# Performance work log

Hardware: AMD Instinct MI355X
Metric: run time of the kernel (lower is better)

The kernel has to match this reference:

```python
import jax, jax.numpy as jnp
import numpy as np
from jax import lax

# Faithful JAX port of the approxmatch CUDA kernel (Fan et al. EMD):
#   iterates annealing levels j = 7 .. -2 with level = -4^j (0 at j=-2),
#   alternately normalizing transport weights by remaining source capacity
#   (remainL) and capping by remaining target capacity (remainR).
# Cost = sum over matched pairs of Euclidean (sqrt) distance * match weight.

def _approx_match(xyz1, xyz2):
    # xyz1: (b,n,3), xyz2: (b,m,3)
    b, n, _ = xyz1.shape
    m = xyz2.shape[1]
    # squared pairwise distances (b,n,m) -- computed once, reused every level
    d2 = jnp.sum((xyz1[:, :, None, :] - xyz2[:, None, :, :]) ** 2, axis=-1)
    # CUDA kernel capacities: multiL = max(1, m/n), multiR = max(1, n/m) (int ratios)
    multiL = float(max(1, m // n))
    multiR = float(max(1, n // m))
    remainL = jnp.full((b, n), multiL, dtype=xyz1.dtype)
    remainR = jnp.full((b, m), multiR, dtype=xyz1.dtype)
    match = jnp.zeros((b, n, m), dtype=xyz1.dtype)

    # levels for j = 7..-1 are -4^j; j = -2 uses level = 0
    levels = jnp.concatenate([
        -(4.0 ** jnp.arange(7, -2, -1, dtype=jnp.float32)),
        jnp.zeros((1,), jnp.float32),
    ])

    def body(carry, level):
        match, remainL, remainR = carry
        w = jnp.exp(level * d2) * remainR[:, None, :]                 # (b,n,m)
        w = w * (remainL / (1e-9 + w.sum(axis=2)))[:, :, None]        # normalize rows, scale by L capacity
        r = jnp.minimum(remainR / (1e-9 + w.sum(axis=1)), 1.0)        # cap columns by R capacity
        w = w * r[:, None, :]
        match = match + w
        remainL = jnp.maximum(remainL - w.sum(axis=2), 0.0)
        remainR = jnp.maximum(remainR - w.sum(axis=1), 0.0)
        return (match, remainL, remainR), None

    (match, _, _), _ = lax.scan(body, (match, remainL, remainR), levels)
    return match, d2


def _match_cost(match, d2):
    # matchcost kernel: sum_{k,l} match[k,l] * sqrt(||xyz1_k - xyz2_l||^2)
    dist = jnp.sqrt(jnp.maximum(d2, 1e-30))
    return jnp.sum(match * dist, axis=(1, 2))  # (b,)


def setup_inputs() -> dict:
    key = jax.random.key(0)
    k1, k2 = jax.random.split(key)
    b, n, m = 8, 2048, 2048
    input1 = jax.random.uniform(k1, (b, n, 3), dtype=jnp.float32)
    input2 = jax.random.uniform(k2, (b, m, 3), dtype=jnp.float32)
    return {"input1": input1, "input2": input2}


def reference(input1, input2):
    match, d2 = _approx_match(input1, input2)
    return _match_cost(match, d2)  # (b,) per-batch EMD cost
```

## Files before the change

### kernel.cpp

```cpp
#include <hip/hip_runtime.h>
#include <math.h>


#define NPTS 2048
#define BLOCK 256
#define RPB 16
#define L2E 1.4426950408889634f

typedef float v2 __attribute__((ext_vector_type(2)));

__device__ __forceinline__ float fexp2(float x) { return __builtin_amdgcn_exp2f(x); }
__device__ __forceinline__ float fsqrt(float x) { return __builtin_amdgcn_sqrtf(x); }
__device__ __forceinline__ v2 fma2(v2 a, v2 b, v2 c) { return __builtin_elementwise_fma(a, b, c); }
__device__ __forceinline__ v2 sp(float a) { v2 r; r.x = a; r.y = a; return r; }
__device__ __forceinline__ float xreduce(float v) {
#pragma unroll
    for (int off = 1; off < 64; off <<= 1) v += __shfl_xor(v, off, 64);
    return v;
}

struct RowPair { v2 pa, px, py, pz; };
__device__ __forceinline__ RowPair mk_pair(float4 a, float4 b, float kp) {
    RowPair r;
    r.pa = v2{kp * a.w, kp * b.w};
    r.px = v2{-2.f*kp*a.x, -2.f*kp*b.x};
    r.py = v2{-2.f*kp*a.y, -2.f*kp*b.y};
    r.pz = v2{-2.f*kp*a.z, -2.f*kp*b.z};
    return r;
}
__device__ __forceinline__ v2 term(const RowPair& r, float qx, float qy, float qz, v2 qb2) {
    return fma2(r.px, sp(qx), fma2(r.py, sp(qy), fma2(r.pz, sp(qz), r.pa + qb2)));
}

__global__ __launch_bounds__(BLOCK) void k_A(
    const float* __restrict__ xyz1, const float* __restrict__ xyz2,
    float4* __restrict__ p1w, float4* __restrict__ p2w,
    float* __restrict__ f_g, float kk, float multiL, float multiR)
{
    __shared__ float4 sQ[NPTS];
    const int row0 = blockIdx.x * RPB;
    const int batch = row0 >> 11;
    const int rloc = row0 & 2047;
    const float* g1 = xyz1 + (size_t)batch * NPTS * 3;
    const float* g2 = xyz2 + (size_t)batch * NPTS * 3;
    if (threadIdx.x < RPB) {
        int i = rloc + threadIdx.x;
        p1w[((size_t)batch << 11) + i] = make_float4(g1[3*i], g1[3*i+1], g1[3*i+2], 0.f);
    } else if (threadIdx.x < 2 * RPB) {
        int i = rloc + threadIdx.x - RPB;
        p2w[((size_t)batch << 11) + i] = make_float4(g2[3*i], g2[3*i+1], g2[3*i+2], 0.f);
    }
    for (int j = threadIdx.x; j < NPTS; j += BLOCK) {
        float qx = g2[3*j], qy = g2[3*j+1], qz = g2[3*j+2];
        sQ[j] = make_float4(qx, qy, qz, kk * (qx*qx + qy*qy + qz*qz));
    }
    __syncthreads();
    const int lane = threadIdx.x & 63;
    const int wave = threadIdx.x >> 6;
    const int r0 = row0 + wave * 4;
    RowPair rA, rB;
    {
        const float* p = g1 + 3 * (r0 & 2047);
        float4 p0 = make_float4(p[0], p[1], p[2], p[0]*p[0]+p[1]*p[1]+p[2]*p[2]);
        float4 p1 = make_float4(p[3], p[4], p[5], p[3]*p[3]+p[4]*p[4]+p[5]*p[5]);
        float4 p2 = make_float4(p[6], p[7], p[8], p[6]*p[6]+p[7]*p[7]+p[8]*p[8]);
        float4 p3 = make_float4(p[9], p[10], p[11], p[9]*p[9]+p[10]*p[10]+p[11]*p[11]);
        rA = mk_pair(p0, p1, kk); rB = mk_pair(p2, p3, kk);
    }
    v2 aSA = sp(0.f), aSB = sp(0.f);
#pragma unroll 8
    for (int j = lane; j < NPTS; j += 64) {
        float4 q = sQ[j];
        v2 qb2 = sp(q.w);
        v2 tA = term(rA, q.x, q.y, q.z, qb2);
        v2 tB = term(rB, q.x, q.y, q.z, qb2);
        aSA += v2{fexp2(tA.x), fexp2(tA.y)};
        aSB += v2{fexp2(tB.x), fexp2(tB.y)};
    }
    float sv[4] = {xreduce(aSA.x), xreduce(aSA.y), xreduce(aSB.x), xreduce(aSB.y)};
    if (lane == 0) {
#pragma unroll
        for (int r = 0; r < 4; ++r)
            f_g[r0 + r] = multiL / (1e-9f + multiR * sv[r]);
    }
}

template <bool FIRST>
__global__ __launch_bounds__(BLOCK) void k_B(
    const float4* __restrict__ p1w, const float4* __restrict__ p2w,
    const float* __restrict__ f_g, float* __restrict__ remR,
    float* __restrict__ c_g, float kk, float multiR)
{
    __shared__ float4 sQ[NPTS];
    __shared__ float sF[NPTS];
    const int col0 = blockIdx.x * RPB;
    const int batch = col0 >> 11;
    const float4* P1 = p1w + ((size_t)batch << 11);
    const float* F = f_g + ((size_t)batch << 11);
    for (int i = threadIdx.x; i < NPTS; i += BLOCK) {
        float4 q = P1[i];
        q.w = kk * (q.x*q.x + q.y*q.y + q.z*q.z);
        sQ[i] = q;
        sF[i] = F[i];
    }
    __syncthreads();
    const int lane = threadIdx.x & 63;
    const int wave = threadIdx.x >> 6;
    const int c0 = col0 + wave * 4;
    RowPair rA, rB;
    {
        float4 q0 = p2w[c0], q1 = p2w[c0+1], q2 = p2w[c0+2], q3 = p2w[c0+3];
        q0.w = q0.x*q0.x + q0.y*q0.y + q0.z*q0.z;
        q1.w = q1.x*q1.x + q1.y*q1.y + q1.z*q1.z;
        q2.w = q2.x*q2.x + q2.y*q2.y + q2.z*q2.z;
        q3.w = q3.x*q3.x + q3.y*q3.y + q3.z*q3.z;
        rA = mk_pair(q0, q1, kk); rB = mk_pair(q2, q3, kk);
    }
    v2 aSA = sp(0.f), aSB = sp(0.f);
#pragma unroll 8
    for (int i = lane; i < NPTS; i += 64) {
        float4 p = sQ[i];
        v2 qb2 = sp(p.w);
        v2 w2 = sp(sF[i]);
        v2 tA = term(rA, p.x, p.y, p.z, qb2);
        v2 tB = term(rB, p.x, p.y, p.z, qb2);
        aSA = fma2(w2, v2{fexp2(tA.x), fexp2(tA.y)}, aSA);
        aSB = fma2(w2, v2{fexp2(tB.x), fexp2(tB.y)}, aSB);
    }
    float sv[4] = {xreduce(aSA.x), xreduce(aSA.y), xreduce(aSB.x), xreduce(aSB.y)};
    if (lane == 0) {
#pragma unroll
        for (int r = 0; r < 4; ++r) {
            int gj = c0 + r;
            float R = FIRST ? multiR : remR[gj];
            float colsum = R * sv[r];
            float rr = fminf(R / (1e-9f + colsum), 1.0f);
            c_g[gj] = R * rr;
            remR[gj] = fmaxf(R - colsum * rr, 0.f);
        }
    }
}

template <int MODE, bool FIRSTC>
__global__ __launch_bounds__(BLOCK) void k_CA(
    const float4* __restrict__ p1w, const float4* __restrict__ p2w,
    float* __restrict__ f_g, const float* __restrict__ c_g,
    const float* __restrict__ remR, float* __restrict__ remL,
    float* __restrict__ costrow, float kp, float rsqkp, float multiL)
{
    __shared__ float4 sQ[NPTS];
    __shared__ float2 sCR[NPTS];
    const int row0 = blockIdx.x * RPB;
    const int batch = row0 >> 11;
    const float4* P2 = p2w + ((size_t)batch << 11);
    const float* C = c_g + ((size_t)batch << 11);
    const float* R = remR + ((size_t)batch << 11);
    for (int j = threadIdx.x; j < NPTS; j += BLOCK) {
        float4 q = P2[j];
        q.w = kp * (q.x*q.x + q.y*q.y + q.z*q.z);
        sQ[j] = q;
        sCR[j] = make_float2(C[j], MODE ? R[j] : 0.f);
    }
    __syncthreads();
    const int lane = threadIdx.x & 63;
    const int wave = threadIdx.x >> 6;
    const int r0 = row0 + wave * 4;

    if (MODE == 0) {
        float px[4], py[4], pz[4], aU[4];
#pragma unroll
        for (int r = 0; r < 4; ++r) {
            float4 q = p1w[r0 + r];
            px[r] = q.x; py[r] = q.y; pz[r] = q.z; aU[r] = 0.f;
        }
        float aT = 0.f;
#pragma unroll 4
        for (int j = lane; j < NPTS; j += 64) {
            float4 q = sQ[j];
            float cw = sCR[j].x;
            aT += cw;
#pragma unroll
            for (int r = 0; r < 4; ++r) {
                float dx = px[r]-q.x, dy = py[r]-q.y, dz = pz[r]-q.z;
                float d2 = fmaf(dx, dx, fmaf(dy, dy, dz * dz));
                aU[r] = fmaf(cw, fsqrt(d2), aU[r]);
            }
        }
        float tt = xreduce(aT);
#pragma unroll
        for (int r = 0; r < 4; ++r) {
            float uu = xreduce(aU[r]);
            if (lane == 0) {
                int gi = r0 + r;
                float fi = f_g[gi];
                remL[gi] = fmaxf(remL[gi] - fi * tt, 0.f);
                costrow[gi] += fi * uu;
            }
        }
        return;
    }

    RowPair rA, rB;
    v2 fiA, fiB;
    {
        float4 p0 = p1w[r0], p1 = p1w[r0+1], p2 = p1w[r0+2], p3 = p1w[r0+3];
        p0.w = p0.x*p0.x + p0.y*p0.y + p0.z*p0.z;
        p1.w = p1.x*p1.x + p1.y*p1.y + p1.z*p1.z;
        p2.w = p2.x*p2.x + p2.y*p2.y + p2.z*p2.z;
        p3.w = p3.x*p3.x + p3.y*p3.y + p3.z*p3.z;
        rA = mk_pair(p0, p1, kp); rB = mk_pair(p2, p3, kp);
        fiA = v2{f_g[r0], f_g[r0+1]}; fiB = v2{f_g[r0+2], f_g[r0+3]};
    }
    v2 aTA = sp(0.f), aTB = sp(0.f), aUA = sp(0.f), aUB = sp(0.f);
    v2 aAA = sp(0.f), aAB = sp(0.f);
    float aAs = 0.f;
#pragma unroll 4
    for (int j = lane; j < NPTS; j += 64) {
        float4 q = sQ[j];
        float2 crj = sCR[j];
        v2 qb2 = sp(q.w);
        float cw = crj.x, rw = crj.y;
        v2 tA = term(rA, q.x, q.y, q.z, qb2);
        v2 tB = term(rB, q.x, q.y, q.z, qb2);
        v2 eA = v2{fexp2(tA.x), fexp2(tA.y)};
        v2 eB = v2{fexp2(tB.x), fexp2(tB.y)};
        v2 eCA, eCB;
        if (MODE == 1) {
            v2 e2A = eA * eA, e2B = eB * eB;
            eCA = sp(cw) * (e2A * e2A); eCB = sp(cw) * (e2B * e2B);
        } else {
            eCA = sp(cw) * eA; eCB = sp(cw) * eB;
        }
        aTA += eCA; aTB += eCB;
        v2 stA = v2{fsqrt(fabsf(tA.x)), fsqrt(fabsf(tA.y))};
        v2 stB = v2{fsqrt(fabsf(tB.x)), fsqrt(fabsf(tB.y))};
        aUA = fma2(eCA, stA, aUA); aUB = fma2(eCB, stB, aUB);
        if (MODE == 1) { aAA = fma2(sp(rw), eA, aAA); aAB = fma2(sp(rw), eB, aAB); }
        else           { aAs += rw; }
    }
    float aas = (MODE == 2) ? xreduce(aAs) : 0.f;
    float tt[4] = {xreduce(aTA.x), xreduce(aTA.y), xreduce(aTB.x), xreduce(aTB.y)};
    float uu[4] = {xreduce(aUA.x), xreduce(aUA.y), xreduce(aUB.x), xreduce(aUB.y)};
    float aav[4];
    if (MODE == 1) {
        aav[0] = xreduce(aAA.x); aav[1] = xreduce(aAA.y);
        aav[2] = xreduce(aAB.x); aav[3] = xreduce(aAB.y);
    } else {
        aav[0] = aav[1] = aav[2] = aav[3] = aas;
    }
    float fiv[4] = {fiA.x, fiA.y, fiB.x, fiB.y};
    if (lane == 0) {
#pragma unroll
        for (int r = 0; r < 4; ++r) {
            int gi = r0 + r;
            float rl0 = FIRSTC ? multiL : remL[gi];
            float rl = fmaxf(rl0 - fiv[r] * tt[r], 0.f);
            costrow[gi] = (FIRSTC ? 0.f : costrow[gi]) + fiv[r] * uu[r] * rsqkp;
            remL[gi] = rl;
            f_g[gi] = rl / (1e-9f + aav[r]);
        }
    }
}

__global__ void k_cost(const float* __restrict__ costrow,
                       float* __restrict__ out, int n) {
    __shared__ float wsum[BLOCK / 64];
    const float* cr = costrow + (size_t)blockIdx.x * n;
    float s = 0.f;
    for (int i = threadIdx.x; i < n; i += BLOCK) s += cr[i];
    s = xreduce(s);
    int wave = threadIdx.x >> 6, lane = threadIdx.x & 63;
    if (lane == 0) wsum[wave] = s;
    __syncthreads();
    if (threadIdx.x == 0) {
        float t = 0.f;
#pragma unroll
        for (int w = 0; w < BLOCK / 64; ++w) t += wsum[w];
        out[blockIdx.x] = t;
    }
}

extern "C" void kernel_launch(void* const* d_in, const int* in_sizes, int n_in,
                              void* d_out, int out_size, void* d_ws, size_t ws_size,
                              hipStream_t stream) {
    const float* xyz1 = (const float*)d_in[0];
    const float* xyz2 = (const float*)d_in[1];
    float* out = (float*)d_out;
    const int b = out_size;
    const int n = in_sizes[0] / (3 * b);
    const int m = in_sizes[1] / (3 * b);
    const int bn = b * n, bm = b * m;

    float4* p1w = (float4*)d_ws;
    float4* p2w = p1w + bn;
    float* remL    = (float*)(p2w + bm);
    float* remR    = remL + bn;
    float* f       = remR + bm;
    float* c       = f + bn;
    float* costrow = c + bm;

    const float multiL = (float)((m / n > 1) ? (m / n) : 1);
    const float multiR = (float)((n / m > 1) ? (n / m) : 1);

    dim3 g(bn / RPB), blk(BLOCK);
    const float kk0 = -16384.f * L2E;
    k_A<<<g, blk, 0, stream>>>(xyz1, xyz2, p1w, p2w, f, kk0, multiL, multiR);

    for (int t = 0; t < 10; ++t) {
        const float lvl = (t < 9) ? -exp2f(2.f * (float)(7 - t)) : 0.f;
        const float kk = lvl * L2E;
        if (t == 0)
            k_B<true><<<g, blk, 0, stream>>>(p1w, p2w, f, remR, c, kk, multiR);
        else
            k_B<false><<<g, blk, 0, stream>>>(p1w, p2w, f, remR, c, kk, multiR);

        if (t < 8) {
            const float kp = kk * 0.25f;
            const float rsq = 1.f / sqrtf(-kp);
            if (t == 0)
                k_CA<1, true><<<g, blk, 0, stream>>>(p1w, p2w, f, c, remR, remL,
                                                     costrow, kp, rsq, multiL);
            else
                k_CA<1, false><<<g, blk, 0, stream>>>(p1w, p2w, f, c, remR, remL,
                                                      costrow, kp, rsq, multiL);
        } else if (t == 8) {
            const float kp = -0.25f * L2E;
            const float rsq = 1.f / sqrtf(0.25f * L2E);
            k_CA<2, false><<<g, blk, 0, stream>>>(p1w, p2w, f, c, remR, remL,
                                                  costrow, kp, rsq, multiL);
        } else {
            k_CA<0, false><<<g, blk, 0, stream>>>(p1w, p2w, f, c, remR, remL,
                                                  costrow, 0.f, 1.f, multiL);
        }
    }
    k_cost<<<dim3(b), blk, 0, stream>>>(costrow, out, n);
}
```

Measured before the change: 280.2 us.

## Process eight rows per wave with software-prefetched LDS loads

Each wave now handles 8 rows or columns instead of 4, and each block covers 32 instead of 16, so every LDS load of a point is reused across more exp/sqrt computations. The inner loops are rewritten as non-unrolled loops that prefetch the next point from shared memory while computing the current one. The grid shrinks by half, which cuts the total LDS staging work but leaves fewer blocks to spread across CUs and raises register pressure.

```diff
diff --git a/kernel.cpp b/kernel.cpp
--- a/kernel.cpp
+++ b/kernel.cpp
@@ -4,7 +4,8 @@
 
 #define NPTS 2048
 #define BLOCK 256
-#define RPB 16
+#define RPW 8
+#define RPB 32
 #define L2E 1.4426950408889634f
 
 typedef float v2 __attribute__((ext_vector_type(2)));
@@ -30,6 +31,10 @@
 }
 __device__ __forceinline__ v2 term(const RowPair& r, float qx, float qy, float qz, v2 qb2) {
     return fma2(r.px, sp(qx), fma2(r.py, sp(qy), fma2(r.pz, sp(qz), r.pa + qb2)));
+}
+__device__ __forceinline__ float4 with_sq(float4 p) {
+    p.w = p.x*p.x + p.y*p.y + p.z*p.z;
+    return p;
 }
 
 __global__ __launch_bounds__(BLOCK) void k_A(
@@ -57,30 +62,40 @@
     __syncthreads();
     const int lane = threadIdx.x & 63;
     const int wave = threadIdx.x >> 6;
-    const int r0 = row0 + wave * 4;
-    RowPair rA, rB;
-    {
-        const float* p = g1 + 3 * (r0 & 2047);
-        float4 p0 = make_float4(p[0], p[1], p[2], p[0]*p[0]+p[1]*p[1]+p[2]*p[2]);
-        float4 p1 = make_float4(p[3], p[4], p[5], p[3]*p[3]+p[4]*p[4]+p[5]*p[5]);
-        float4 p2 = make_float4(p[6], p[7], p[8], p[6]*p[6]+p[7]*p[7]+p[8]*p[8]);
-        float4 p3 = make_float4(p[9], p[10], p[11], p[9]*p[9]+p[10]*p[10]+p[11]*p[11]);
-        rA = mk_pair(p0, p1, kk); rB = mk_pair(p2, p3, kk);
-    }
-    v2 aSA = sp(0.f), aSB = sp(0.f);
-#pragma unroll 8
-    for (int j = lane; j < NPTS; j += 64) {
-        float4 q = sQ[j];
-        v2 qb2 = sp(q.w);
-        v2 tA = term(rA, q.x, q.y, q.z, qb2);
-        v2 tB = term(rB, q.x, q.y, q.z, qb2);
-        aSA += v2{fexp2(tA.x), fexp2(tA.y)};
-        aSB += v2{fexp2(tB.x), fexp2(tB.y)};
-    }
-    float sv[4] = {xreduce(aSA.x), xreduce(aSA.y), xreduce(aSB.x), xreduce(aSB.y)};
+    const int r0 = row0 + wave * RPW;
+    RowPair rp[4];
+#pragma unroll
+    for (int k = 0; k < 4; ++k) {
+        const float* p = g1 + 3 * ((r0 & 2047) + 2 * k);
+        float4 a = make_float4(p[0], p[1], p[2], p[0]*p[0]+p[1]*p[1]+p[2]*p[2]);
+        float4 b = make_float4(p[3], p[4], p[5], p[3]*p[3]+p[4]*p[4]+p[5]*p[5]);
+        rp[k] = mk_pair(a, b, kk);
+    }
+    v2 aS[4];
+#pragma unroll
+    for (int k = 0; k < 4; ++k) aS[k] = sp(0.f);
+    float4 qc = sQ[lane];
+#pragma unroll 1
+    for (int it = 0; it < NPTS / 64; ++it) {
+        float4 qn = sQ[(lane + (it + 1) * 64) & 2047];
+        v2 qb2 = sp(qc.w);
+#pragma unroll
+        for (int k = 0; k < 4; ++k) {
+            v2 t = term(rp[k], qc.x, qc.y, qc.z, qb2);
+            aS[k] += v2{fexp2(t.x), fexp2(t.y)};
+        }
+        qc = qn;
+    }
+    if (lane == 0) {  }
+    float sv[RPW];
+#pragma unroll
+    for (int k = 0; k < 4; ++k) {
+        sv[2*k]   = xreduce(aS[k].x);
+        sv[2*k+1] = xreduce(aS[k].y);
+    }
     if (lane == 0) {
 #pragma unroll
-        for (int r = 0; r < 4; ++r)
+        for (int r = 0; r < RPW; ++r)
             f_g[r0 + r] = multiL / (1e-9f + multiR * sv[r]);
     }
 }
@@ -106,31 +121,39 @@
     __syncthreads();
     const int lane = threadIdx.x & 63;
     const int wave = threadIdx.x >> 6;
-    const int c0 = col0 + wave * 4;
-    RowPair rA, rB;
-    {
-        float4 q0 = p2w[c0], q1 = p2w[c0+1], q2 = p2w[c0+2], q3 = p2w[c0+3];
-        q0.w = q0.x*q0.x + q0.y*q0.y + q0.z*q0.z;
-        q1.w = q1.x*q1.x + q1.y*q1.y + q1.z*q1.z;
-        q2.w = q2.x*q2.x + q2.y*q2.y + q2.z*q2.z;
-        q3.w = q3.x*q3.x + q3.y*q3.y + q3.z*q3.z;
-        rA = mk_pair(q0, q1, kk); rB = mk_pair(q2, q3, kk);
-    }
-    v2 aSA = sp(0.f), aSB = sp(0.f);
-#pragma unroll 8
-    for (int i = lane; i < NPTS; i += 64) {
-        float4 p = sQ[i];
-        v2 qb2 = sp(p.w);
-        v2 w2 = sp(sF[i]);
-        v2 tA = term(rA, p.x, p.y, p.z, qb2);
-        v2 tB = term(rB, p.x, p.y, p.z, qb2);
-        aSA = fma2(w2, v2{fexp2(tA.x), fexp2(tA.y)}, aSA);
-        aSB = fma2(w2, v2{fexp2(tB.x), fexp2(tB.y)}, aSB);
-    }
-    float sv[4] = {xreduce(aSA.x), xreduce(aSA.y), xreduce(aSB.x), xreduce(aSB.y)};
+    const int c0 = col0 + wave * RPW;
+    RowPair rp[4];
+#pragma unroll
+    for (int k = 0; k < 4; ++k)
+        rp[k] = mk_pair(with_sq(p2w[c0 + 2*k]), with_sq(p2w[c0 + 2*k + 1]), kk);
+    v2 aS[4];
+#pragma unroll
+    for (int k = 0; k < 4; ++k) aS[k] = sp(0.f);
+    float4 qc = sQ[lane];
+    float fc = sF[lane];
+#pragma unroll 1
+    for (int it = 0; it < NPTS / 64; ++it) {
+        int jn = (lane + (it + 1) * 64) & 2047;
+        float4 qn = sQ[jn];
+        float fn = sF[jn];
+        v2 qb2 = sp(qc.w);
+        v2 w2 = sp(fc);
+#pragma unroll
+        for (int k = 0; k < 4; ++k) {
+            v2 t = term(rp[k], qc.x, qc.y, qc.z, qb2);
+            aS[k] = fma2(w2, v2{fexp2(t.x), fexp2(t.y)}, aS[k]);
+        }
+        qc = qn; fc = fn;
+    }
+    float sv[RPW];
+#pragma unroll
+    for (int k = 0; k < 4; ++k) {
+        sv[2*k]   = xreduce(aS[k].x);
+        sv[2*k+1] = xreduce(aS[k].y);
+    }
     if (lane == 0) {
 #pragma unroll
-        for (int r = 0; r < 4; ++r) {
+        for (int r = 0; r < RPW; ++r) {
             int gj = c0 + r;
             float R = FIRST ? multiR : remR[gj];
             float colsum = R * sv[r];
@@ -164,31 +187,35 @@
     __syncthreads();
     const int lane = threadIdx.x & 63;
     const int wave = threadIdx.x >> 6;
-    const int r0 = row0 + wave * 4;
+    const int r0 = row0 + wave * RPW;
 
     if (MODE == 0) {
-        float px[4], py[4], pz[4], aU[4];
-#pragma unroll
-        for (int r = 0; r < 4; ++r) {
+        float px[RPW], py[RPW], pz[RPW], aU[RPW];
+#pragma unroll
+        for (int r = 0; r < RPW; ++r) {
             float4 q = p1w[r0 + r];
             px[r] = q.x; py[r] = q.y; pz[r] = q.z; aU[r] = 0.f;
         }
         float aT = 0.f;
-#pragma unroll 4
-        for (int j = lane; j < NPTS; j += 64) {
-            float4 q = sQ[j];
-            float cw = sCR[j].x;
-            aT += cw;
-#pragma unroll
-            for (int r = 0; r < 4; ++r) {
-                float dx = px[r]-q.x, dy = py[r]-q.y, dz = pz[r]-q.z;
+        float4 qc = sQ[lane];
+        float cwc = sCR[lane].x;
+#pragma unroll 1
+        for (int it = 0; it < NPTS / 64; ++it) {
+            int jn = (lane + (it + 1) * 64) & 2047;
+            float4 qn = sQ[jn];
+            float cwn = sCR[jn].x;
+            aT += cwc;
+#pragma unroll
+            for (int r = 0; r < RPW; ++r) {
+                float dx = px[r]-qc.x, dy = py[r]-qc.y, dz = pz[r]-qc.z;
                 float d2 = fmaf(dx, dx, fmaf(dy, dy, dz * dz));
-                aU[r] = fmaf(cw, fsqrt(d2), aU[r]);
+                aU[r] = fmaf(cwc, fsqrt(d2), aU[r]);
             }
+            qc = qn; cwc = cwn;
         }
         float tt = xreduce(aT);
 #pragma unroll
-        for (int r = 0; r < 4; ++r) {
+        for (int r = 0; r < RPW; ++r) {
             float uu = xreduce(aU[r]);
             if (lane == 0) {
                 int gi = r0 + r;
@@ -200,58 +227,53 @@
         return;
     }
 
-    RowPair rA, rB;
-    v2 fiA, fiB;
-    {
-        float4 p0 = p1w[r0], p1 = p1w[r0+1], p2 = p1w[r0+2], p3 = p1w[r0+3];
-        p0.w = p0.x*p0.x + p0.y*p0.y + p0.z*p0.z;
-        p1.w = p1.x*p1.x + p1.y*p1.y + p1.z*p1.z;
-        p2.w = p2.x*p2.x + p2.y*p2.y + p2.z*p2.z;
-        p3.w = p3.x*p3.x + p3.y*p3.y + p3.z*p3.z;
-        rA = mk_pair(p0, p1, kp); rB = mk_pair(p2, p3, kp);
-        fiA = v2{f_g[r0], f_g[r0+1]}; fiB = v2{f_g[r0+2], f_g[r0+3]};
-    }
-    v2 aTA = sp(0.f), aTB = sp(0.f), aUA = sp(0.f), aUB = sp(0.f);
-    v2 aAA = sp(0.f), aAB = sp(0.f);
+    RowPair rp[4];
+    float fiv[RPW];
+#pragma unroll
+    for (int k = 0; k < 4; ++k) {
+        rp[k] = mk_pair(with_sq(p1w[r0 + 2*k]), with_sq(p1w[r0 + 2*k + 1]), kp);
+        fiv[2*k] = f_g[r0 + 2*k]; fiv[2*k+1] = f_g[r0 + 2*k + 1];
+    }
+    v2 aT[4], aU[4], aA[4];
+#pragma unroll
+    for (int k = 0; k < 4; ++k) { aT[k] = sp(0.f); aU[k] = sp(0.f); aA[k] = sp(0.f); }
     float aAs = 0.f;
-#pragma unroll 4
-    for (int j = lane; j < NPTS; j += 64) {
-        float4 q = sQ[j];
-        float2 crj = sCR[j];
-        v2 qb2 = sp(q.w);
-        float cw = crj.x, rw = crj.y;
-        v2 tA = term(rA, q.x, q.y, q.z, qb2);
-        v2 tB = term(rB, q.x, q.y, q.z, qb2);
-        v2 eA = v2{fexp2(tA.x), fexp2(tA.y)};
-        v2 eB = v2{fexp2(tB.x), fexp2(tB.y)};
-        v2 eCA, eCB;
-        if (MODE == 1) {
-            v2 e2A = eA * eA, e2B = eB * eB;
-            eCA = sp(cw) * (e2A * e2A); eCB = sp(cw) * (e2B * e2B);
-        } else {
-            eCA = sp(cw) * eA; eCB = sp(cw) * eB;
-        }
-        aTA += eCA; aTB += eCB;
-        v2 stA = v2{fsqrt(fabsf(tA.x)), fsqrt(fabsf(tA.y))};
-        v2 stB = v2{fsqrt(fabsf(tB.x)), fsqrt(fabsf(tB.y))};
-        aUA = fma2(eCA, stA, aUA); aUB = fma2(eCB, stB, aUB);
-        if (MODE == 1) { aAA = fma2(sp(rw), eA, aAA); aAB = fma2(sp(rw), eB, aAB); }
-        else           { aAs += rw; }
+    float4 qc = sQ[lane];
+    float2 crc = sCR[lane];
+#pragma unroll 1
+    for (int it = 0; it < NPTS / 64; ++it) {
+        int jn = (lane + (it + 1) * 64) & 2047;
+        float4 qn = sQ[jn];
+        float2 crn = sCR[jn];
+        v2 qb2 = sp(qc.w);
+        float cw = crc.x, rw = crc.y;
+        if (MODE == 2) aAs += rw;
+#pragma unroll
+        for (int k = 0; k < 4; ++k) {
+            v2 t = term(rp[k], qc.x, qc.y, qc.z, qb2);
+            v2 e = v2{fexp2(t.x), fexp2(t.y)};
+            v2 eC;
+            if (MODE == 1) { v2 e2 = e * e; eC = sp(cw) * (e2 * e2); }
+            else           { eC = sp(cw) * e; }
+            aT[k] += eC;
+            v2 st = v2{fsqrt(fabsf(t.x)), fsqrt(fabsf(t.y))};
+            aU[k] = fma2(eC, st, aU[k]);
+            if (MODE == 1) aA[k] = fma2(sp(rw), e, aA[k]);
+        }
+        qc = qn; crc = crn;
     }
     float aas = (MODE == 2) ? xreduce(aAs) : 0.f;
-    float tt[4] = {xreduce(aTA.x), xreduce(aTA.y), xreduce(aTB.x), xreduce(aTB.y)};
-    float uu[4] = {xreduce(aUA.x), xreduce(aUA.y), xreduce(aUB.x), xreduce(aUB.y)};
-    float aav[4];
-    if (MODE == 1) {
-        aav[0] = xreduce(aAA.x); aav[1] = xreduce(aAA.y);
-        aav[2] = xreduce(aAB.x); aav[3] = xreduce(aAB.y);
-    } else {
-        aav[0] = aav[1] = aav[2] = aav[3] = aas;
-    }
-    float fiv[4] = {fiA.x, fiA.y, fiB.x, fiB.y};
+    float tt[RPW], uu[RPW], aav[RPW];
+#pragma unroll
+    for (int k = 0; k < 4; ++k) {
+        tt[2*k]   = xreduce(aT[k].x);  tt[2*k+1] = xreduce(aT[k].y);
+        uu[2*k]   = xreduce(aU[k].x);  uu[2*k+1] = xreduce(aU[k].y);
+        if (MODE == 1) { aav[2*k] = xreduce(aA[k].x); aav[2*k+1] = xreduce(aA[k].y); }
+        else           { aav[2*k] = aas; aav[2*k+1] = aas; }
+    }
     if (lane == 0) {
 #pragma unroll
-        for (int r = 0; r < 4; ++r) {
+        for (int r = 0; r < RPW; ++r) {
             int gi = r0 + r;
             float rl0 = FIRSTC ? multiL : remL[gi];
             float rl = fmaxf(rl0 - fiv[r] * tt[r], 0.f);
```

Result: slower. 292.2 us (+4.3%).

## Fold row weights into exponent and specialize final zero-level pass

Applied to the files above, without the earlier changes.

In k_B, each row factor f is folded into the exponent as log2(f) in the shared point's w component, which removes the shared sF array and one multiply per element. At the last level (level 0) every exp term is 1, so the column pass becomes a per-batch sum of f. That replaces the O(n·m) k_B launch with a small reduction kernel, k_B9. The final cost pass, k_C9, also adds in costrow and accumulates per-batch output with atomics, which removes the separate k_cost launch. Risks are log2 of a zero or tiny f producing -inf (which still gives exp2 = 0), atomic ordering nondeterminism, and the MODE 0 remL update being dropped because it is unused afterward.

```diff
diff --git a/kernel.cpp b/kernel.cpp
--- a/kernel.cpp
+++ b/kernel.cpp
@@ -11,6 +11,7 @@
 
 __device__ __forceinline__ float fexp2(float x) { return __builtin_amdgcn_exp2f(x); }
 __device__ __forceinline__ float fsqrt(float x) { return __builtin_amdgcn_sqrtf(x); }
+__device__ __forceinline__ float flog2(float x) { return __builtin_amdgcn_logf(x); }
 __device__ __forceinline__ v2 fma2(v2 a, v2 b, v2 c) { return __builtin_elementwise_fma(a, b, c); }
 __device__ __forceinline__ v2 sp(float a) { v2 r; r.x = a; r.y = a; return r; }
 __device__ __forceinline__ float xreduce(float v) {
@@ -30,6 +31,10 @@
 }
 __device__ __forceinline__ v2 term(const RowPair& r, float qx, float qy, float qz, v2 qb2) {
     return fma2(r.px, sp(qx), fma2(r.py, sp(qy), fma2(r.pz, sp(qz), r.pa + qb2)));
+}
+__device__ __forceinline__ float4 with_sq(float4 p) {
+    p.w = p.x*p.x + p.y*p.y + p.z*p.z;
+    return p;
 }
 
 __global__ __launch_bounds__(BLOCK) void k_A(
@@ -92,16 +97,14 @@
     float* __restrict__ c_g, float kk, float multiR)
 {
     __shared__ float4 sQ[NPTS];
-    __shared__ float sF[NPTS];
     const int col0 = blockIdx.x * RPB;
     const int batch = col0 >> 11;
     const float4* P1 = p1w + ((size_t)batch << 11);
     const float* F = f_g + ((size_t)batch << 11);
     for (int i = threadIdx.x; i < NPTS; i += BLOCK) {
         float4 q = P1[i];
-        q.w = kk * (q.x*q.x + q.y*q.y + q.z*q.z);
+        q.w = kk * (q.x*q.x + q.y*q.y + q.z*q.z) + flog2(F[i]);
         sQ[i] = q;
-        sF[i] = F[i];
     }
     __syncthreads();
     const int lane = threadIdx.x & 63;
@@ -109,11 +112,8 @@
     const int c0 = col0 + wave * 4;
     RowPair rA, rB;
     {
-        float4 q0 = p2w[c0], q1 = p2w[c0+1], q2 = p2w[c0+2], q3 = p2w[c0+3];
-        q0.w = q0.x*q0.x + q0.y*q0.y + q0.z*q0.z;
-        q1.w = q1.x*q1.x + q1.y*q1.y + q1.z*q1.z;
-        q2.w = q2.x*q2.x + q2.y*q2.y + q2.z*q2.z;
-        q3.w = q3.x*q3.x + q3.y*q3.y + q3.z*q3.z;
+        float4 q0 = with_sq(p2w[c0]),     q1 = with_sq(p2w[c0+1]);
+        float4 q2 = with_sq(p2w[c0+2]),   q3 = with_sq(p2w[c0+3]);
         rA = mk_pair(q0, q1, kk); rB = mk_pair(q2, q3, kk);
     }
     v2 aSA = sp(0.f), aSB = sp(0.f);
@@ -121,11 +121,10 @@
     for (int i = lane; i < NPTS; i += 64) {
         float4 p = sQ[i];
         v2 qb2 = sp(p.w);
-        v2 w2 = sp(sF[i]);
         v2 tA = term(rA, p.x, p.y, p.z, qb2);
         v2 tB = term(rB, p.x, p.y, p.z, qb2);
-        aSA = fma2(w2, v2{fexp2(tA.x), fexp2(tA.y)}, aSA);
-        aSB = fma2(w2, v2{fexp2(tB.x), fexp2(tB.y)}, aSB);
+        aSA += v2{fexp2(tA.x), fexp2(tA.y)};
+        aSB += v2{fexp2(tB.x), fexp2(tB.y)};
     }
     float sv[4] = {xreduce(aSA.x), xreduce(aSA.y), xreduce(aSB.x), xreduce(aSB.y)};
     if (lane == 0) {
@@ -138,6 +137,30 @@
             c_g[gj] = R * rr;
             remR[gj] = fmaxf(R - colsum * rr, 0.f);
         }
+    }
+}
+
+__global__ __launch_bounds__(BLOCK) void k_B9(
+    const float* __restrict__ f_g, const float* __restrict__ remR,
+    float* __restrict__ c_g, float* __restrict__ out)
+{
+    __shared__ float wsum[BLOCK / 64];
+    const int batch = blockIdx.x;
+    const float* F = f_g + ((size_t)batch << 11);
+    float s = 0.f;
+    for (int i = threadIdx.x; i < NPTS; i += BLOCK) s += F[i];
+    s = xreduce(s);
+    int wave = threadIdx.x >> 6, lane = threadIdx.x & 63;
+    if (lane == 0) wsum[wave] = s;
+    __syncthreads();
+    float Ftot = (wsum[0] + wsum[1]) + (wsum[2] + wsum[3]);
+    if (threadIdx.x == 0) out[batch] = 0.f;
+    for (int j = threadIdx.x; j < NPTS; j += BLOCK) {
+        int gj = (batch << 11) + j;
+        float R = remR[gj];
+        float colsum = R * Ftot;
+        float rr = fminf(R / (1e-9f + colsum), 1.0f);
+        c_g[gj] = R * rr;
     }
 }
 
@@ -159,55 +182,18 @@
         float4 q = P2[j];
         q.w = kp * (q.x*q.x + q.y*q.y + q.z*q.z);
         sQ[j] = q;
-        sCR[j] = make_float2(C[j], MODE ? R[j] : 0.f);
+        sCR[j] = make_float2(C[j], R[j]);
     }
     __syncthreads();
     const int lane = threadIdx.x & 63;
     const int wave = threadIdx.x >> 6;
     const int r0 = row0 + wave * 4;
 
-    if (MODE == 0) {
-        float px[4], py[4], pz[4], aU[4];
-#pragma unroll
-        for (int r = 0; r < 4; ++r) {
-            float4 q = p1w[r0 + r];
-            px[r] = q.x; py[r] = q.y; pz[r] = q.z; aU[r] = 0.f;
-        }
-        float aT = 0.f;
-#pragma unroll 4
-        for (int j = lane; j < NPTS; j += 64) {
-            float4 q = sQ[j];
-            float cw = sCR[j].x;
-            aT += cw;
-#pragma unroll
-            for (int r = 0; r < 4; ++r) {
-                float dx = px[r]-q.x, dy = py[r]-q.y, dz = pz[r]-q.z;
-                float d2 = fmaf(dx, dx, fmaf(dy, dy, dz * dz));
-                aU[r] = fmaf(cw, fsqrt(d2), aU[r]);
-            }
-        }
-        float tt = xreduce(aT);
-#pragma unroll
-        for (int r = 0; r < 4; ++r) {
-            float uu = xreduce(aU[r]);
-            if (lane == 0) {
-                int gi = r0 + r;
-                float fi = f_g[gi];
-                remL[gi] = fmaxf(remL[gi] - fi * tt, 0.f);
-                costrow[gi] += fi * uu;
-            }
-        }
-        return;
-    }
-
     RowPair rA, rB;
     v2 fiA, fiB;
     {
-        float4 p0 = p1w[r0], p1 = p1w[r0+1], p2 = p1w[r0+2], p3 = p1w[r0+3];
-        p0.w = p0.x*p0.x + p0.y*p0.y + p0.z*p0.z;
-        p1.w = p1.x*p1.x + p1.y*p1.y + p1.z*p1.z;
-        p2.w = p2.x*p2.x + p2.y*p2.y + p2.z*p2.z;
-        p3.w = p3.x*p3.x + p3.y*p3.y + p3.z*p3.z;
+        float4 p0 = with_sq(p1w[r0]),   p1 = with_sq(p1w[r0+1]);
+        float4 p2 = with_sq(p1w[r0+2]), p3 = with_sq(p1w[r0+3]);
         rA = mk_pair(p0, p1, kp); rB = mk_pair(p2, p3, kp);
         fiA = v2{f_g[r0], f_g[r0+1]}; fiB = v2{f_g[r0+2], f_g[r0+3]};
     }
@@ -262,22 +248,53 @@
     }
 }
 
-__global__ void k_cost(const float* __restrict__ costrow,
-                       float* __restrict__ out, int n) {
+__global__ __launch_bounds__(BLOCK) void k_C9(
+    const float4* __restrict__ p1w, const float4* __restrict__ p2w,
+    const float* __restrict__ f_g, const float* __restrict__ c_g,
+    const float* __restrict__ costrow, float* __restrict__ out)
+{
+    __shared__ float4 sQ[NPTS];
+    __shared__ float sC[NPTS];
     __shared__ float wsum[BLOCK / 64];
-    const float* cr = costrow + (size_t)blockIdx.x * n;
-    float s = 0.f;
-    for (int i = threadIdx.x; i < n; i += BLOCK) s += cr[i];
-    s = xreduce(s);
-    int wave = threadIdx.x >> 6, lane = threadIdx.x & 63;
-    if (lane == 0) wsum[wave] = s;
-    __syncthreads();
-    if (threadIdx.x == 0) {
-        float t = 0.f;
-#pragma unroll
-        for (int w = 0; w < BLOCK / 64; ++w) t += wsum[w];
-        out[blockIdx.x] = t;
-    }
+    const int row0 = blockIdx.x * RPB;
+    const int batch = row0 >> 11;
+    const float4* P2 = p2w + ((size_t)batch << 11);
+    const float* C = c_g + ((size_t)batch << 11);
+    for (int j = threadIdx.x; j < NPTS; j += BLOCK) {
+        sQ[j] = P2[j];
+        sC[j] = C[j];
+    }
+    __syncthreads();
+    const int lane = threadIdx.x & 63;
+    const int wave = threadIdx.x >> 6;
+    const int r0 = row0 + wave * 4;
+    float px[4], py[4], pz[4], aU[4];
+#pragma unroll
+    for (int r = 0; r < 4; ++r) {
+        float4 q = p1w[r0 + r];
+        px[r] = q.x; py[r] = q.y; pz[r] = q.z; aU[r] = 0.f;
+    }
+#pragma unroll 4
+    for (int j = lane; j < NPTS; j += 64) {
+        float4 q = sQ[j];
+        float cw = sC[j];
+#pragma unroll
+        for (int r = 0; r < 4; ++r) {
+            float dx = px[r]-q.x, dy = py[r]-q.y, dz = pz[r]-q.z;
+            float d2 = fmaf(dx, dx, fmaf(dy, dy, dz * dz));
+            aU[r] = fmaf(cw, fsqrt(d2), aU[r]);
+        }
+    }
+    float psum = 0.f;
+#pragma unroll
+    for (int r = 0; r < 4; ++r) {
+        float uu = xreduce(aU[r]);
+        if (lane == 0) psum += costrow[r0 + r] + f_g[r0 + r] * uu;
+    }
+    if (lane == 0) wsum[wave] = psum;
+    __syncthreads();
+    if (threadIdx.x == 0)
+        atomicAdd(&out[batch], (wsum[0] + wsum[1]) + (wsum[2] + wsum[3]));
 }
 
 extern "C" void kernel_launch(void* const* d_in, const int* in_sizes, int n_in,
@@ -306,9 +323,8 @@
     const float kk0 = -16384.f * L2E;
     k_A<<<g, blk, 0, stream>>>(xyz1, xyz2, p1w, p2w, f, kk0, multiL, multiR);
 
-    for (int t = 0; t < 10; ++t) {
-        const float lvl = (t < 9) ? -exp2f(2.f * (float)(7 - t)) : 0.f;
-        const float kk = lvl * L2E;
+    for (int t = 0; t < 9; ++t) {
+        const float kk = -exp2f(2.f * (float)(7 - t)) * L2E;
         if (t == 0)
             k_B<true><<<g, blk, 0, stream>>>(p1w, p2w, f, remR, c, kk, multiR);
         else
@@ -323,15 +339,13 @@
             else
                 k_CA<1, false><<<g, blk, 0, stream>>>(p1w, p2w, f, c, remR, remL,
                                                       costrow, kp, rsq, multiL);
-        } else if (t == 8) {
+        } else {
             const float kp = -0.25f * L2E;
             const float rsq = 1.f / sqrtf(0.25f * L2E);
             k_CA<2, false><<<g, blk, 0, stream>>>(p1w, p2w, f, c, remR, remL,
                                                   costrow, kp, rsq, multiL);
-        } else {
-            k_CA<0, false><<<g, blk, 0, stream>>>(p1w, p2w, f, c, remR, remL,
-                                                  costrow, 0.f, 1.f, multiL);
-        }
-    }
-    k_cost<<<dim3(b), blk, 0, stream>>>(costrow, out, n);
-}
+        }
+    }
+    k_B9<<<dim3(b), blk, 0, stream>>>(f, remR, c, out);
+    k_C9<<<g, blk, 0, stream>>>(p1w, p2w, f, c, costrow, out);
+}
```

New measurement: 276.2 us, median of 2. About the same (-1.4%).
